# Kernel tuning notes

Hardware: AMD Instinct MI355X
Metric: run time of the kernel (lower is better)

Reference implementation:

```python
import math
import jax, jax.numpy as jnp
import numpy as np

L, B, D, Z, H, N = 2048, 8, 1024, 128, 2048, 16
MAXPOS = 2048
LAPLACE_MU, LAPLACE_SIGMA = 0.707107, 0.282095


def setup_inputs() -> dict:
    key = jax.random.key(0)
    ks = jax.random.split(key, 14)
    def rn(k, shp, s=1.0):
        return jax.random.normal(k, shp, dtype=jnp.float32) * s
    return {
        "x": rn(ks[0], (L, B, D)),
        # MultiHeadEMA params (unidirectional: kernel_dim == D)
        "delta": rn(ks[1], (D, N, 1), 0.2),
        "alpha": rn(ks[2], (D, N, 1), 0.2),
        "beta_ema": rn(ks[3], (D, N, 1), 0.02) + 1.0,
        "gamma_ema": rn(ks[4], (D, N)),
        "omega": rn(ks[5], (D,)),
        # projections
        "v_w": rn(ks[6], (D, H), 0.02), "v_b": jnp.zeros((H,), jnp.float32),
        "mx_w": rn(ks[7], (D, Z + H + 2 * D), 0.02),
        "mx_b": jnp.zeros((Z + H + 2 * D,), jnp.float32),
        "h_w": rn(ks[8], (H, D), 0.02), "h_b": jnp.zeros((D,), jnp.float32),
        # q/k affine from shared z
        "qk_gamma": rn(ks[9], (2, Z), 0.1) + 1.0,
        "qk_beta": rn(ks[10], (2, Z), 0.1),
        # simple relative positional bias
        "rel_pos": rn(ks[11], (2 * MAXPOS - 1,), 0.02),
        # prenorm layernorm
        "ln_w": jnp.ones((D,), jnp.float32),
        "ln_b": jnp.zeros((D,), jnp.float32),
    }


def _laplace(x):
    x = (x - LAPLACE_MU) / (LAPLACE_SIGMA * math.sqrt(2.0))
    return 0.5 * (1.0 + jax.lax.erf(x))


def _layer_norm(x, w, b, eps=1e-5):
    mu = jnp.mean(x, axis=-1, keepdims=True)
    var = jnp.mean(jnp.square(x - mu), axis=-1, keepdims=True)
    return (x - mu) * jax.lax.rsqrt(var + eps) * w + b


def _rel_bias(rel_pos, seq_len):
    # SimpleRelativePositionalBias: Toeplitz (L, L) matrix from a 2L-1 vector
    bvec = rel_pos[MAXPOS - seq_len:MAXPOS + seq_len - 1]  # (2L-1,)
    t = jnp.pad(bvec, (0, seq_len))                         # (3L-1,)
    t = jnp.tile(t, seq_len)[:-seq_len].reshape(seq_len, 3 * seq_len - 2)
    r = (2 * seq_len - 1) // 2
    return t[:, r:t.shape[1] - r]                           # (L, L)


def _ema_conv(xn, delta, alpha, beta_ema, gamma_ema, omega, seq_len):
    # xn: (L, B, D) -> silu(EMA(xn) + xn * omega), via FFT convolution
    scale = 1.0 / math.sqrt(N)
    p = jax.nn.sigmoid(delta)                 # (D, N, 1)
    q = 1.0 - p * jax.nn.sigmoid(alpha)       # (D, N, 1)
    vander = jnp.arange(seq_len, dtype=jnp.float32)[None, None, :] * jnp.log(q)  # (D, N, L)
    kernel = jnp.einsum('dnl,dn->dl', p * beta_ema * jnp.exp(vander), gamma_ema * scale)  # (D, L)
    residual = xn * omega                     # (L, B, D)
    xt = jnp.transpose(xn, (1, 2, 0))         # (B, D, L)
    nfft = 2 * seq_len
    kf = jnp.fft.rfft(kernel, n=nfft)         # (D, L+1) complex
    xf = jnp.fft.rfft(xt, n=nfft)             # (B, D, L+1)
    out = jnp.fft.irfft(xf * kf, n=nfft)[..., :seq_len]  # (B, D, L)
    return jax.nn.silu(jnp.transpose(out, (2, 0, 1)) + residual)  # (L, B, D)


def reference(x, delta, alpha, beta_ema, gamma_ema, omega,
              v_w, v_b, mx_w, mx_b, h_w, h_b,
              qk_gamma, qk_beta, rel_pos, ln_w, ln_b):
    seq_len = x.shape[0]
    residual = x
    xn = _layer_norm(x, ln_w, ln_b)                       # prenorm
    v = jax.nn.silu(xn @ v_w + v_b)                        # (L, B, H)
    mx = _ema_conv(xn, delta, alpha, beta_ema, gamma_ema, omega, seq_len)  # (L, B, D)
    base = mx @ mx_w + mx_b                                # (L, B, D+Z+H+D)
    u = jax.nn.sigmoid(base[..., :D])                      # update gate (L, B, D)
    zr = jax.nn.silu(base[..., D:D + Z + H])
    hx = base[..., D + Z + H:]                             # (L, B, D)
    z = zr[..., :Z]                                        # (L, B, Z)
    r = zr[..., Z:]                                        # (L, B, H)
    zqk = z[..., None, :] * qk_gamma + qk_beta             # (L, B, 2, Z)
    q = jnp.transpose(zqk[..., 0, :], (1, 0, 2))           # (B, L, Z)
    k = jnp.transpose(zqk[..., 1, :], (1, 0, 2))           # (B, L, Z)
    vb = jnp.transpose(v, (1, 0, 2))                       # (B, L, H)
    bias = _rel_bias(rel_pos, seq_len)                     # (L, L)
    qk = jnp.einsum('blz,bmz->blm', q, k) / seq_len + bias # (B, L, L)
    attn = _laplace(qk)
    h = jnp.einsum('blm,bmh->blh', attn, vb)               # (B, L, H)
    h = jnp.transpose(h, (1, 0, 2))                        # (L, B, H)
    h = jax.nn.silu(hx + (h * r) @ h_w + h_b)              # (L, B, D)
    out = residual + u * (h - residual)
    return out
```

## Files before the change

kernel.cpp:

```cpp
#include <hip/hip_runtime.h>
#include <hip/hip_bf16.h>
#include <math.h>

typedef unsigned short u16;
typedef unsigned int   u32;
typedef __bf16 bf16x8_t __attribute__((ext_vector_type(8)));
typedef float  f32x4_t  __attribute__((ext_vector_type(4)));

#define DEVI static __device__ __forceinline__

DEVI float bf2f(u16 u){ union{u32 i; float f;} v; v.i = ((u32)u)<<16; return v.f; }
DEVI u16 f2bf(float f){ union{float f; u32 i;} v; v.f = f; u32 i = v.i; i += 0x7fffu + ((i>>16)&1u); return (u16)(i>>16); }
DEVI float sigm(float x){ return 1.0f/(1.0f + __expf(-x)); }
DEVI float silu_(float x){ return x * sigm(x); }

DEVI void gload16(const u16* gsrc, u16* lds){
  __builtin_amdgcn_global_load_lds(
      (const __attribute__((address_space(1))) unsigned int*)gsrc,
      (__attribute__((address_space(3))) unsigned int*)lds, 16, 0, 0);
}

constexpr int L_=2048, B_=8, D_=1024, Z_=128, H_=2048, N_=16;
constexpr int CH_=128, NC_=16;
constexpr int MXN_=4224, MXNP_=4352;

__global__ __launch_bounds__(256) void k_ln(const float* __restrict__ x,
                                            const float* __restrict__ w,
                                            const float* __restrict__ b,
                                            u16* __restrict__ xn){
  int row = blockIdx.x, t = threadIdx.x;
  int l = row >> 3, bb = row & 7;
  const float4* xr = (const float4*)(x + (size_t)row*D_);
  float4 v = xr[t];
  float s  = v.x+v.y+v.z+v.w;
  float sq = v.x*v.x+v.y*v.y+v.z*v.z+v.w*v.w;
  #pragma unroll
  for (int m=1; m<64; m<<=1){ s += __shfl_xor(s, m); sq += __shfl_xor(sq, m); }
  __shared__ float ss[4], sv[4];
  int wv = t>>6;
  if ((t&63)==0){ ss[wv]=s; sv[wv]=sq; }
  __syncthreads();
  s = ss[0]+ss[1]+ss[2]+ss[3]; sq = sv[0]+sv[1]+sv[2]+sv[3];
  float mu = s*(1.0f/D_);
  float var = sq*(1.0f/D_) - mu*mu;
  float rs = rsqrtf(var + 1e-5f);
  float4 wv4 = ((const float4*)w)[t];
  float4 bv4 = ((const float4*)b)[t];
  u16 o0 = f2bf((v.x-mu)*rs*wv4.x+bv4.x);
  u16 o1 = f2bf((v.y-mu)*rs*wv4.y+bv4.y);
  u16 o2 = f2bf((v.z-mu)*rs*wv4.z+bv4.z);
  u16 o3 = f2bf((v.w-mu)*rs*wv4.w+bv4.w);
  *(uint2*)(xn + ((size_t)bb*L_ + l)*D_ + t*4) =
      make_uint2((u32)o0 | ((u32)o1<<16), (u32)o2 | ((u32)o3<<16));
}

__global__ __launch_bounds__(256) void k_tr(const float* __restrict__ in, int R, int C,
                                            u16* __restrict__ out){
  __shared__ u16 TT[32*33];
  int c0 = blockIdx.x*32, r0 = blockIdx.y*32;
  int t = threadIdx.x;
  int lr = t>>3, lc4 = (t&7)*4;
  float4 v = *(const float4*)&in[(size_t)(r0+lr)*C + c0 + lc4];
  TT[(lc4+0)*33 + lr] = f2bf(v.x);
  TT[(lc4+1)*33 + lr] = f2bf(v.y);
  TT[(lc4+2)*33 + lr] = f2bf(v.z);
  TT[(lc4+3)*33 + lr] = f2bf(v.w);
  __syncthreads();
  int orr = t>>3, oc4 = (t&7)*4;
  u16 a0 = TT[orr*33 + oc4+0], a1 = TT[orr*33 + oc4+1];
  u16 a2 = TT[orr*33 + oc4+2], a3 = TT[orr*33 + oc4+3];
  *(uint2*)&out[(size_t)(c0+orr)*R + r0 + oc4] =
      make_uint2((u32)a0 | ((u32)a1<<16), (u32)a2 | ((u32)a3<<16));
}

__global__ void k_ema_params(const float* __restrict__ delta, const float* __restrict__ alpha,
                             const float* __restrict__ beta,  const float* __restrict__ gamma,
                             float* __restrict__ qA, float* __restrict__ wcA, float* __restrict__ qPA){
  int i = blockIdx.x*256 + threadIdx.x;
  if (i >= D_*N_) return;
  float p = 1.0f/(1.0f + expf(-delta[i]));
  float q = 1.0f - p*(1.0f/(1.0f + expf(-alpha[i])));
  qA[i]  = q;
  wcA[i] = p*beta[i]*gamma[i]*0.25f;
  qPA[i] = powf(q, (float)CH_);
}

__global__ __launch_bounds__(256) void k_ema_a(const u16* __restrict__ xn,
                                               const float* __restrict__ qA,
                                               float* __restrict__ F){
  int d = blockIdx.x*256 + threadIdx.x;
  int b = blockIdx.y, c = blockIdx.z;
  float q[N_], s[N_];
  #pragma unroll
  for (int n=0;n<N_;n++){ q[n]=qA[d*N_+n]; s[n]=0.0f; }
  for (int t=0;t<CH_;t++){
    int l = c*CH_ + t;
    float x = bf2f(xn[((size_t)b*L_ + l)*D_ + d]);
    #pragma unroll
    for (int n=0;n<N_;n++) s[n] = q[n]*s[n] + x;
  }
  float* Fo = F + (((size_t)c*B_ + b)*D_ + d)*N_;
  #pragma unroll
  for (int n=0;n<N_;n++) Fo[n] = s[n];
}

__global__ __launch_bounds__(256) void k_ema_b(float* __restrict__ F,
                                               const float* __restrict__ qPA){
  int i = blockIdx.x*256 + threadIdx.x;
  int n = i & (N_-1);
  int d = (i>>4) & (D_-1);
  int b = i >> 14;
  float qP = qPA[d*N_+n];
  float S = 0.0f;
  for (int c=0;c<NC_;c++){
    size_t idx = (((size_t)c*B_ + b)*D_ + d)*N_ + n;
    float f = F[idx];
    F[idx] = S;
    S = qP*S + f;
  }
}

__global__ __launch_bounds__(256) void k_ema_c(const u16* __restrict__ xn,
                                               const float* __restrict__ qA,
                                               const float* __restrict__ wcA,
                                               const float* __restrict__ CY,
                                               const float* __restrict__ omega,
                                               u16* __restrict__ mx){
  int d = blockIdx.x*256 + threadIdx.x;
  int b = blockIdx.y, c = blockIdx.z;
  float q[N_], wc[N_], s[N_];
  const float* cy = CY + (((size_t)c*B_ + b)*D_ + d)*N_;
  #pragma unroll
  for (int n=0;n<N_;n++){ q[n]=qA[d*N_+n]; wc[n]=wcA[d*N_+n]; s[n]=cy[n]; }
  float om = omega[d];
  for (int t=0;t<CH_;t++){
    int l = c*CH_ + t;
    float x = bf2f(xn[((size_t)b*L_ + l)*D_ + d]);
    float acc = 0.0f;
    #pragma unroll
    for (int n=0;n<N_;n++){ s[n] = q[n]*s[n] + x; acc += wc[n]*s[n]; }
    mx[((size_t)b*L_ + l)*D_ + d] = f2bf(silu_(acc + x*om));
  }
}

#define STG2(BUF, K0) do {                                                        \
    int _ab = (BUF)*32768;                                                        \
    _Pragma("unroll")                                                             \
    for (int it=0; it<2; ++it){                                                   \
      int idx = it*1024 + tid; int r = idx>>3, ch = idx&7;                        \
      gload16(Ab + (size_t)(rowBase + r)*lda + (K0) + ((ch ^ (r&7))*8),           \
              &LDS[_ab + idx*8]);                                                 \
    }                                                                             \
    _Pragma("unroll")                                                             \
    for (int it=0; it<2; ++it){                                                   \
      int idx = it*1024 + tid; int r = idx>>3, ch = idx&7;                        \
      gload16(Bb + (size_t)(colBase + r)*ldb + (K0) + ((ch ^ (r&7))*8),           \
              &LDS[_ab + 16384 + idx*8]);                                         \
    }                                                                             \
  } while(0)

#define CMP2(BUF) do {                                                            \
    int _ab = (BUF)*32768;                                                        \
    _Pragma("unroll")                                                             \
    for (int ks=0; ks<2; ++ks){                                                   \
      bf16x8_t af[4], bfr[4];                                                     \
      int kfx = (ks*32 + lane4*8) ^ ((lane15&7)<<3);                              \
      _Pragma("unroll")                                                           \
      for (int m=0;m<4;m++)                                                       \
        af[m]  = *(const bf16x8_t*)&LDS[_ab + (wr*64 + m*16 + lane15)*64 + kfx];  \
      _Pragma("unroll")                                                           \
      for (int n=0;n<4;n++)                                                       \
        bfr[n] = *(const bf16x8_t*)&LDS[_ab + 16384 + (wc*64 + n*16 + lane15)*64 + kfx]; \
      __builtin_amdgcn_s_setprio(1);                                              \
      _Pragma("unroll")                                                           \
      for (int m=0;m<4;m++)                                                       \
        _Pragma("unroll")                                                         \
        for (int n=0;n<4;n++)                                                     \
          acc[m][n] = __builtin_amdgcn_mfma_f32_16x16x32_bf16(af[m], bfr[n], acc[m][n], 0,0,0); \
      __builtin_amdgcn_s_setprio(0);                                              \
    }                                                                             \
  } while(0)

template<int OP>
__global__ __launch_bounds__(1024, 4) void k_g2(
    const u16* __restrict__ A, int lda, long aStr,
    const u16* __restrict__ Bm, int ldb, long bStr,
    int K,
    u16* __restrict__ C, int ldc, long cStr,
    const float* __restrict__ biasC, const float* __restrict__ biasR,
    const float* __restrict__ qkg, const float* __restrict__ qkb,
    u16* __restrict__ P0, u16* __restrict__ P1,
    u16* __restrict__ P2, u16* __restrict__ P3,
    const u16* __restrict__ RP0)
{
  __shared__ u16 LDS[65536];
  int zz = blockIdx.z;
  const u16* Ab = A + (size_t)zz*aStr;
  const u16* Bb = Bm + (size_t)zz*bStr;

  int gx = gridDim.x;
  int f = blockIdx.x + gx*blockIdx.y;
  int q8 = (gx*gridDim.y) >> 3;
  int wg = (f & 7)*q8 + (f >> 3);
  int rowBase = (wg / gx)*256;
  int colBase = (wg % gx)*256;

  int tid = threadIdx.x;
  int lane = tid & 63, wave = tid >> 6;
  int wr = wave >> 2, wc = wave & 3;
  int lane15 = lane & 15, lane4 = lane >> 4;

  f32x4_t acc[4][4];
  #pragma unroll
  for (int m=0;m<4;m++)
    #pragma unroll
    for (int n=0;n<4;n++) acc[m][n] = (f32x4_t){0.f,0.f,0.f,0.f};

  int nt = K >> 6;
  STG2(0, 0);
  STG2(1, 64);
  for (int t = 0; t < nt; ++t){
    if (t + 1 < nt) { asm volatile("s_waitcnt vmcnt(4)" ::: "memory"); }
    else            { asm volatile("s_waitcnt vmcnt(0)" ::: "memory"); }
    __builtin_amdgcn_s_barrier();
    __builtin_amdgcn_sched_barrier(0);
    CMP2(t & 1);
    if (t + 2 < nt) {
      __builtin_amdgcn_s_barrier();
      STG2(t & 1, (t+2)*64);
    }
  }

  u16* Cb  = C  ? C  + (size_t)zz*cStr : nullptr;
  u16* P0b = P0 ? P0 + (size_t)zz*((size_t)L_*D_) : nullptr;
  u16* P1b = P1 ? P1 + (size_t)zz*((size_t)L_*D_) : nullptr;
  u16* P2b = P2 ? P2 + (size_t)zz*((size_t)L_*Z_) : nullptr;
  u16* P3b = P3 ? P3 + (size_t)zz*((size_t)L_*Z_) : nullptr;
  const u16* RP0b = RP0 ? RP0 + (size_t)zz*((size_t)L_*H_) : nullptr;

  #pragma unroll
  for (int m=0;m<4;m++) {
    #pragma unroll
    for (int n=0;n<4;n++) {
      int col = colBase + wc*64 + n*16 + lane15;
      #pragma unroll
      for (int r2=0;r2<4;r2++) {
        int row = rowBase + wr*64 + m*16 + lane4*4 + r2;
        float v = acc[m][n][r2];
        if (OP == 0) {
          Cb[(size_t)row*ldc + col] = f2bf(silu_(v + biasR[row]));
        } else if (OP == 1) {
          if (col < MXN_) {
            v += biasC[col];
            if (col < 1024) {
              P0b[(size_t)row*1024 + col] = f2bf(sigm(v));
            } else if (col < 1152) {
              float s = silu_(v);
              int zi = col - 1024;
              P2b[(size_t)row*128 + zi] = f2bf(s*qkg[zi]     + qkb[zi]);
              P3b[(size_t)row*128 + zi] = f2bf(s*qkg[128+zi] + qkb[128+zi]);
            } else if (col < 3200) {
              Cb[(size_t)row*2048 + (col-1152)] = f2bf(silu_(v));
            } else {
              P1b[(size_t)row*1024 + (col-3200)] = f2bf(v);
            }
          }
        } else {
          v *= bf2f(RP0b[(size_t)row*ldc + col]);
          Cb[(size_t)row*ldc + col] = f2bf(v);
        }
      }
    }
  }
}

#define STG(BUF, K0) do {                                                         \
    int _ab = (BUF)*16384;                                                        \
    _Pragma("unroll")                                                             \
    for (int it=0; it<4; ++it){                                                   \
      int idx = it*256 + tid; int r = idx>>3, ch = idx&7;                         \
      gload16(Ab + (size_t)(rowBase + r)*lda + (K0) + ((ch ^ (r&7))*8),           \
              &LDS[_ab + idx*8]);                                                 \
    }                                                                             \
    _Pragma("unroll")                                                             \
    for (int it=0; it<4; ++it){                                                   \
      int idx = it*256 + tid; int r = idx>>3, ch = idx&7;                         \
      gload16(Bb + (size_t)(colBase + r)*ldb + (K0) + ((ch ^ (r&7))*8),           \
              &LDS[_ab + 8192 + idx*8]);                                          \
    }                                                                             \
  } while(0)

#define CMP(BUF) do {                                                             \
    int _ab = (BUF)*16384;                                                        \
    _Pragma("unroll")                                                             \
    for (int ks=0; ks<2; ++ks){                                                   \
      bf16x8_t af[4], bfr[4];                                                     \
      int kfx = (ks*32 + lane4*8) ^ ((lane15&7)<<3);                              \
      _Pragma("unroll")                                                           \
      for (int m=0;m<4;m++)                                                       \
        af[m]  = *(const bf16x8_t*)&LDS[_ab + (wm + m*16 + lane15)*64 + kfx];     \
      _Pragma("unroll")                                                           \
      for (int n=0;n<4;n++)                                                       \
        bfr[n] = *(const bf16x8_t*)&LDS[_ab + 8192 + (wn + n*16 + lane15)*64 + kfx]; \
      __builtin_amdgcn_s_setprio(1);                                              \
      _Pragma("unroll")                                                           \
      for (int m=0;m<4;m++)                                                       \
        _Pragma("unroll")                                                         \
        for (int n=0;n<4;n++)                                                     \
          acc[m][n] = __builtin_amdgcn_mfma_f32_16x16x32_bf16(af[m], bfr[n], acc[m][n], 0,0,0); \
      __builtin_amdgcn_s_setprio(0);                                              \
    }                                                                             \
  } while(0)

template<int OP>
__global__ __launch_bounds__(256) void k_gall(
    const u16* __restrict__ A, int lda, long aStr,
    const u16* __restrict__ Bm, int ldb, long bStr,
    int K,
    u16* __restrict__ C, int ldc, long cStr,
    const float* __restrict__ biasC,
    const float* __restrict__ relpos,
    const u16* __restrict__ RP0, const u16* __restrict__ RP1,
    const float* __restrict__ xin, float* __restrict__ outf, int bb)
{
  __shared__ u16 LDS[32768];
  int zz = blockIdx.z;
  const u16* Ab = A + (size_t)zz*aStr;
  const u16* Bb = Bm + (size_t)zz*bStr;

  int gx = gridDim.x;
  int f = blockIdx.x + gx*blockIdx.y;
  int q8 = (gx*gridDim.y) >> 3;
  int wg = (f & 7)*q8 + (f >> 3);
  int rowBase = (wg / gx)*128;
  int colBase = (wg % gx)*128;

  int tid = threadIdx.x;
  int lane = tid & 63, wave = tid >> 6;
  int wm = (wave>>1)*64, wn = (wave&1)*64;
  int lane15 = lane & 15, lane4 = lane >> 4;

  f32x4_t acc[4][4];
  #pragma unroll
  for (int m=0;m<4;m++)
    #pragma unroll
    for (int n=0;n<4;n++) acc[m][n] = (f32x4_t){0.f,0.f,0.f,0.f};

  int nt = K >> 6;
  STG(0, 0);
  STG(1, 64);
  for (int t = 0; t < nt; ++t){
    if (t + 1 < nt) { asm volatile("s_waitcnt vmcnt(8)" ::: "memory"); }
    else            { asm volatile("s_waitcnt vmcnt(0)" ::: "memory"); }
    __builtin_amdgcn_s_barrier();
    __builtin_amdgcn_sched_barrier(0);
    CMP(t & 1);
    if (t + 2 < nt) {
      __builtin_amdgcn_s_barrier();
      STG(t & 1, (t+2)*64);
    }
  }

  u16* Cb = C ? C + (size_t)zz*cStr : nullptr;
  const u16* RP0b = RP0 ? RP0 + (size_t)zz*((size_t)L_*D_) : nullptr;
  const u16* RP1b = RP1 ? RP1 + (size_t)zz*((size_t)L_*D_) : nullptr;
  int bglob = bb + zz;

  #pragma unroll
  for (int m=0;m<4;m++) {
    #pragma unroll
    for (int n=0;n<4;n++) {
      int col = colBase + wn + n*16 + lane15;
      #pragma unroll
      for (int r2=0;r2<4;r2++) {
        int row = rowBase + wm + m*16 + lane4*4 + r2;
        float v = acc[m][n][r2];
        if (OP == 2) {
          v = v*(1.0f/(float)L_) + relpos[2047 + col - row];
          v = 0.5f*(1.0f + erff((v - 0.707107f)*2.5066282746f));
          Cb[(size_t)row*ldc + col] = f2bf(v);
        } else {
          v += biasC[col];
          float hx = bf2f(RP0b[(size_t)row*1024 + col]);
          float hval = silu_(hx + v);
          size_t gi = ((size_t)row*B_ + bglob)*D_ + col;
          float xv = xin[gi];
          float uu = bf2f(RP1b[(size_t)row*1024 + col]);
          outf[gi] = xv + uu*(hval - xv);
        }
      }
    }
  }
}

extern "C" void kernel_launch(void* const* d_in, const int* in_sizes, int n_in,
                              void* d_out, int out_size, void* d_ws, size_t ws_size,
                              hipStream_t stream) {
  const float* x      = (const float*)d_in[0];
  const float* delta  = (const float*)d_in[1];
  const float* alpha  = (const float*)d_in[2];
  const float* betaE  = (const float*)d_in[3];
  const float* gammaE = (const float*)d_in[4];
  const float* omega  = (const float*)d_in[5];
  const float* v_w    = (const float*)d_in[6];
  const float* v_b    = (const float*)d_in[7];
  const float* mx_w   = (const float*)d_in[8];
  const float* mx_b   = (const float*)d_in[9];
  const float* h_w    = (const float*)d_in[10];
  const float* h_b    = (const float*)d_in[11];
  const float* qkg    = (const float*)d_in[12];
  const float* qkb    = (const float*)d_in[13];
  const float* relpos = (const float*)d_in[14];
  const float* ln_w   = (const float*)d_in[15];
  const float* ln_b   = (const float*)d_in[16];
  float* out = (float*)d_out;

  const size_t fixedB = 92995584ull;
  const size_t perNB  = 42991616ull;
  int NB = 8;
  while (NB > 1 && fixedB + (size_t)NB*perNB > ws_size) NB >>= 1;
  int NG = B_ / NB;

  char* ws = (char*)d_ws;
  size_t o = 0;
  auto alloc = [&](size_t sz){ size_t r = o; o += sz; return r; };
  u16* XN    = (u16*)(ws + alloc(33554432));
  u16* MX    = (u16*)(ws + alloc(33554432));
  u16* VWT   = (u16*)(ws + alloc(4194304));
  u16* MXWT  = (u16*)(ws + alloc((size_t)MXNP_*D_*2));
  u16* HWT   = (u16*)(ws + alloc(4194304));
  float* EQ  = (float*)(ws + alloc(65536));
  float* EW  = (float*)(ws + alloc(65536));
  float* EP  = (float*)(ws + alloc(65536));
  float* Ff  = (float*)(ws + alloc(8388608));
  u16* VT    = (u16*)(ws + alloc((size_t)NB*8388608));
  u16* ATTN  = (u16*)(ws + alloc((size_t)NB*8388608));
  u16* Rb    = (u16*)(ws + alloc((size_t)NB*8388608));
  u16* HRb   = (u16*)(ws + alloc((size_t)NB*8388608));
  u16* Ub    = (u16*)(ws + alloc((size_t)NB*4194304));
  u16* HXb   = (u16*)(ws + alloc((size_t)NB*4194304));
  u16* Qb    = (u16*)(ws + alloc((size_t)NB*524288));
  u16* Kb    = (u16*)(ws + alloc((size_t)NB*524288));

  k_ln<<<L_*B_, 256, 0, stream>>>(x, ln_w, ln_b, XN);
  k_ema_params<<<(D_*N_+255)/256, 256, 0, stream>>>(delta, alpha, betaE, gammaE, EQ, EW, EP);
  k_ema_a<<<dim3(D_/256, B_, NC_), 256, 0, stream>>>(XN, EQ, Ff);
  k_ema_b<<<(B_*D_*N_)/256, 256, 0, stream>>>(Ff, EP);
  k_ema_c<<<dim3(D_/256, B_, NC_), 256, 0, stream>>>(XN, EQ, EW, Ff, omega, MX);
  k_tr<<<dim3(H_/32, D_/32), 256, 0, stream>>>(v_w, D_, H_, VWT);
  k_tr<<<dim3(MXN_/32, D_/32), 256, 0, stream>>>(mx_w, D_, MXN_, MXWT);
  k_tr<<<dim3(D_/32, H_/32), 256, 0, stream>>>(h_w, H_, D_, HWT);

  for (int g = 0; g < NG; ++g) {
    int b0 = g*NB;
    k_g2<0><<<dim3(L_/256, H_/256, NB), 1024, 0, stream>>>(
        VWT, D_, 0L, XN + (size_t)b0*L_*D_, D_, (long)L_*D_, D_,
        VT, L_, (long)H_*L_,
        nullptr, v_b, nullptr, nullptr,
        nullptr, nullptr, nullptr, nullptr, nullptr);
    k_g2<1><<<dim3(MXNP_/256, L_/256, NB), 1024, 0, stream>>>(
        MX + (size_t)b0*L_*D_, D_, (long)L_*D_, MXWT, D_, 0L, D_,
        Rb, H_, (long)L_*H_,
        mx_b, nullptr, qkg, qkb,
        Ub, HXb, Qb, Kb, nullptr);
    k_gall<2><<<dim3(L_/128, L_/128, NB), 256, 0, stream>>>(
        Qb, Z_, (long)L_*Z_, Kb, Z_, (long)L_*Z_, Z_,
        ATTN, L_, (long)L_*L_,
        nullptr, relpos, nullptr, nullptr, nullptr, nullptr, 0);
    k_g2<3><<<dim3(H_/256, L_/256, NB), 1024, 0, stream>>>(
        ATTN, L_, (long)L_*L_, VT, L_, (long)H_*L_, L_,
        HRb, H_, (long)L_*H_,
        nullptr, nullptr, nullptr, nullptr,
        nullptr, nullptr, nullptr, nullptr, Rb);
    k_gall<4><<<dim3(D_/128, L_/128, NB), 256, 0, stream>>>(
        HRb, H_, (long)L_*H_, HWT, H_, 0L, H_,
        nullptr, 0, 0L,
        h_b, nullptr, HXb, Ub, x, out, b0);
  }
}
```

Baseline: 745.5 us.

## Use 8-wave 256x256 GEMM blocks with 128x64 per-wave tiles

The 256x256 bf16 GEMM kernel moves from 16 waves (1024 threads, 64x64 per wave) to 8 waves (512 threads, 128x64 per wave). Each wave holds 32 accumulator tiles in explicitly named registers, generated by macro lists. Each wave now reuses each B fragment across more rows, which cuts LDS reads per MFMA. The costs are much higher register pressure, lower occupancy (launch bounds 512,2) and twice as many global-to-LDS loads issued per thread, with the vmcnt wait adjusted to match.

```diff
diff --git a/kernel.cpp b/kernel.cpp
--- a/kernel.cpp
+++ b/kernel.cpp
@@ -143,46 +143,93 @@
   }
 }
 
-#define STG2(BUF, K0) do {                                                        \
+template<int OP>
+DEVI void epi_store(int row0, int col, f32x4_t v4,
+                    u16* Cb, int ldc,
+                    u16* P0b, u16* P1b, u16* P2b, u16* P3b,
+                    const u16* RP0b,
+                    const float* biasC, const float* biasR,
+                    const float* qkg, const float* qkb){
+  #pragma unroll
+  for (int r2=0;r2<4;r2++){
+    int row = row0 + r2;
+    float v = v4[r2];
+    if (OP == 0) {
+      Cb[(size_t)row*ldc + col] = f2bf(silu_(v + biasR[row]));
+    } else if (OP == 1) {
+      if (col < MXN_) {
+        v += biasC[col];
+        if (col < 1024) {
+          P0b[(size_t)row*1024 + col] = f2bf(sigm(v));
+        } else if (col < 1152) {
+          float s = silu_(v);
+          int zi = col - 1024;
+          P2b[(size_t)row*128 + zi] = f2bf(s*qkg[zi]     + qkb[zi]);
+          P3b[(size_t)row*128 + zi] = f2bf(s*qkg[128+zi] + qkb[128+zi]);
+        } else if (col < 3200) {
+          Cb[(size_t)row*2048 + (col-1152)] = f2bf(silu_(v));
+        } else {
+          P1b[(size_t)row*1024 + (col-3200)] = f2bf(v);
+        }
+      }
+    } else {
+      v *= bf2f(RP0b[(size_t)row*ldc + col]);
+      Cb[(size_t)row*ldc + col] = f2bf(v);
+    }
+  }
+}
+
+#define ACC_LIST(X) \
+  X(0,0) X(0,1) X(0,2) X(0,3)  X(1,0) X(1,1) X(1,2) X(1,3) \
+  X(2,0) X(2,1) X(2,2) X(2,3)  X(3,0) X(3,1) X(3,2) X(3,3) \
+  X(4,0) X(4,1) X(4,2) X(4,3)  X(5,0) X(5,1) X(5,2) X(5,3) \
+  X(6,0) X(6,1) X(6,2) X(6,3)  X(7,0) X(7,1) X(7,2) X(7,3)
+#define AF_LIST(X) X(0) X(1) X(2) X(3) X(4) X(5) X(6) X(7)
+#define BF_LIST(X) X(0) X(1) X(2) X(3)
+
+#define DECL_ACC(M,N) f32x4_t A_##M##_##N = (f32x4_t){0.f,0.f,0.f,0.f};
+#define MFMA_STEP(M,N) A_##M##_##N = __builtin_amdgcn_mfma_f32_16x16x32_bf16(AF##M, BF##N, A_##M##_##N, 0,0,0);
+#define LD_AF(M) bf16x8_t AF##M = *(const bf16x8_t*)&LDS[_ab + (wr*128 + M*16 + lane15)*64 + kfx];
+#define LD_BF(N) bf16x8_t BF##N = *(const bf16x8_t*)&LDS[_ab + 16384 + (wc*64 + N*16 + lane15)*64 + kfx];
+#define EPI_ST(M,N) epi_store<OP>(rowBase + wr*128 + M*16 + lane4*4, \
+                                  colBase + wc*64 + N*16 + lane15, A_##M##_##N, \
+                                  Cb, ldc, P0b, P1b, P2b, P3b, RP0b, biasC, biasR, qkg, qkb);
+
+#define STG8(BUF, K0) do {                                                        \
     int _ab = (BUF)*32768;                                                        \
     _Pragma("unroll")                                                             \
-    for (int it=0; it<2; ++it){                                                   \
-      int idx = it*1024 + tid; int r = idx>>3, ch = idx&7;                        \
+    for (int it=0; it<4; ++it){                                                   \
+      int idx = it*512 + tid; int r = idx>>3, ch = idx&7;                         \
       gload16(Ab + (size_t)(rowBase + r)*lda + (K0) + ((ch ^ (r&7))*8),           \
               &LDS[_ab + idx*8]);                                                 \
     }                                                                             \
     _Pragma("unroll")                                                             \
-    for (int it=0; it<2; ++it){                                                   \
-      int idx = it*1024 + tid; int r = idx>>3, ch = idx&7;                        \
+    for (int it=0; it<4; ++it){                                                   \
+      int idx = it*512 + tid; int r = idx>>3, ch = idx&7;                         \
       gload16(Bb + (size_t)(colBase + r)*ldb + (K0) + ((ch ^ (r&7))*8),           \
               &LDS[_ab + 16384 + idx*8]);                                         \
     }                                                                             \
   } while(0)
 
-#define CMP2(BUF) do {                                                            \
+#define CMP8(BUF) do {                                                            \
     int _ab = (BUF)*32768;                                                        \
-    _Pragma("unroll")                                                             \
-    for (int ks=0; ks<2; ++ks){                                                   \
-      bf16x8_t af[4], bfr[4];                                                     \
-      int kfx = (ks*32 + lane4*8) ^ ((lane15&7)<<3);                              \
-      _Pragma("unroll")                                                           \
-      for (int m=0;m<4;m++)                                                       \
-        af[m]  = *(const bf16x8_t*)&LDS[_ab + (wr*64 + m*16 + lane15)*64 + kfx];  \
-      _Pragma("unroll")                                                           \
-      for (int n=0;n<4;n++)                                                       \
-        bfr[n] = *(const bf16x8_t*)&LDS[_ab + 16384 + (wc*64 + n*16 + lane15)*64 + kfx]; \
+    int _sw = (lane15&7)<<3;                                                      \
+    { int kfx = (lane4*8) ^ _sw;                                                  \
+      AF_LIST(LD_AF)  BF_LIST(LD_BF)                                              \
       __builtin_amdgcn_s_setprio(1);                                              \
-      _Pragma("unroll")                                                           \
-      for (int m=0;m<4;m++)                                                       \
-        _Pragma("unroll")                                                         \
-        for (int n=0;n<4;n++)                                                     \
-          acc[m][n] = __builtin_amdgcn_mfma_f32_16x16x32_bf16(af[m], bfr[n], acc[m][n], 0,0,0); \
+      ACC_LIST(MFMA_STEP)                                                         \
       __builtin_amdgcn_s_setprio(0);                                              \
     }                                                                             \
+    { int kfx = (32 + lane4*8) ^ _sw;                                             \
+      AF_LIST(LD_AF)  BF_LIST(LD_BF)                                              \
+      __builtin_amdgcn_s_setprio(1);                                              \
+      ACC_LIST(MFMA_STEP)                                                         \
+      __builtin_amdgcn_s_setprio(0);                                              \
+    }                                                                             \
   } while(0)
 
 template<int OP>
-__global__ __launch_bounds__(1024, 4) void k_g2(
+__global__ __launch_bounds__(512, 2) void k_g8(
     const u16* __restrict__ A, int lda, long aStr,
     const u16* __restrict__ Bm, int ldb, long bStr,
     int K,
@@ -210,24 +257,20 @@
   int wr = wave >> 2, wc = wave & 3;
   int lane15 = lane & 15, lane4 = lane >> 4;
 
-  f32x4_t acc[4][4];
-  #pragma unroll
-  for (int m=0;m<4;m++)
-    #pragma unroll
-    for (int n=0;n<4;n++) acc[m][n] = (f32x4_t){0.f,0.f,0.f,0.f};
+  ACC_LIST(DECL_ACC)
 
   int nt = K >> 6;
-  STG2(0, 0);
-  STG2(1, 64);
+  STG8(0, 0);
+  STG8(1, 64);
   for (int t = 0; t < nt; ++t){
-    if (t + 1 < nt) { asm volatile("s_waitcnt vmcnt(4)" ::: "memory"); }
+    if (t + 1 < nt) { asm volatile("s_waitcnt vmcnt(8)" ::: "memory"); }
     else            { asm volatile("s_waitcnt vmcnt(0)" ::: "memory"); }
     __builtin_amdgcn_s_barrier();
     __builtin_amdgcn_sched_barrier(0);
-    CMP2(t & 1);
+    CMP8(t & 1);
     if (t + 2 < nt) {
       __builtin_amdgcn_s_barrier();
-      STG2(t & 1, (t+2)*64);
+      STG8(t & 1, (t+2)*64);
     }
   }
 
@@ -238,40 +281,7 @@
   u16* P3b = P3 ? P3 + (size_t)zz*((size_t)L_*Z_) : nullptr;
   const u16* RP0b = RP0 ? RP0 + (size_t)zz*((size_t)L_*H_) : nullptr;
 
-  #pragma unroll
-  for (int m=0;m<4;m++) {
-    #pragma unroll
-    for (int n=0;n<4;n++) {
-      int col = colBase + wc*64 + n*16 + lane15;
-      #pragma unroll
-      for (int r2=0;r2<4;r2++) {
-        int row = rowBase + wr*64 + m*16 + lane4*4 + r2;
-        float v = acc[m][n][r2];
-        if (OP == 0) {
-          Cb[(size_t)row*ldc + col] = f2bf(silu_(v + biasR[row]));
-        } else if (OP == 1) {
-          if (col < MXN_) {
-            v += biasC[col];
-            if (col < 1024) {
-              P0b[(size_t)row*1024 + col] = f2bf(sigm(v));
-            } else if (col < 1152) {
-              float s = silu_(v);
-              int zi = col - 1024;
-              P2b[(size_t)row*128 + zi] = f2bf(s*qkg[zi]     + qkb[zi]);
-              P3b[(size_t)row*128 + zi] = f2bf(s*qkg[128+zi] + qkb[128+zi]);
-            } else if (col < 3200) {
-              Cb[(size_t)row*2048 + (col-1152)] = f2bf(silu_(v));
-            } else {
-              P1b[(size_t)row*1024 + (col-3200)] = f2bf(v);
-            }
-          }
-        } else {
-          v *= bf2f(RP0b[(size_t)row*ldc + col]);
-          Cb[(size_t)row*ldc + col] = f2bf(v);
-        }
-      }
-    }
-  }
+  ACC_LIST(EPI_ST)
 }
 
 #define STG(BUF, K0) do {                                                         \
@@ -453,12 +463,12 @@
 
   for (int g = 0; g < NG; ++g) {
     int b0 = g*NB;
-    k_g2<0><<<dim3(L_/256, H_/256, NB), 1024, 0, stream>>>(
+    k_g8<0><<<dim3(L_/256, H_/256, NB), 512, 0, stream>>>(
         VWT, D_, 0L, XN + (size_t)b0*L_*D_, D_, (long)L_*D_, D_,
         VT, L_, (long)H_*L_,
         nullptr, v_b, nullptr, nullptr,
         nullptr, nullptr, nullptr, nullptr, nullptr);
-    k_g2<1><<<dim3(MXNP_/256, L_/256, NB), 1024, 0, stream>>>(
+    k_g8<1><<<dim3(MXNP_/256, L_/256, NB), 512, 0, stream>>>(
         MX + (size_t)b0*L_*D_, D_, (long)L_*D_, MXWT, D_, 0L, D_,
         Rb, H_, (long)L_*H_,
         mx_b, nullptr, qkg, qkb,
@@ -467,7 +477,7 @@
         Qb, Z_, (long)L_*Z_, Kb, Z_, (long)L_*Z_, Z_,
         ATTN, L_, (long)L_*L_,
         nullptr, relpos, nullptr, nullptr, nullptr, nullptr, 0);
-    k_g2<3><<<dim3(H_/256, L_/256, NB), 1024, 0, stream>>>(
+    k_g8<3><<<dim3(H_/256, L_/256, NB), 512, 0, stream>>>(
         ATTN, L_, (long)L_*L_, VT, L_, (long)H_*L_, L_,
         HRb, H_, (long)L_*H_,
         nullptr, nullptr, nullptr, nullptr,
```

After: 810.9 us. +8.8%, slower.
